# Kernel tuning notes

Hardware: AMD Instinct MI355X
Metric: run time of the kernel (lower is better)

## Reference

```python
import jax, jax.numpy as jnp
import numpy as np

VOCAB, EMB, UNITS, B, S = 32000, 256, 512, 32, 512


def _lstm_scan(x_bse, h0, c0, W, U, b):
    """Keras-order LSTM (gates i,f,g,o). x_bse: [B,S,E]. Returns (out [B,S,U], hT, cT)."""
    # Precompute input projections for all timesteps: [B,S,4U] -> [S,B,4U]
    zx = jnp.einsum('bse,eu->bsu', x_bse, W) + b
    zx = jnp.swapaxes(zx, 0, 1)

    def step(carry, zt):
        h, c = carry
        z = zt + h @ U  # [B,4U]
        i, f, g, o = jnp.split(z, 4, axis=-1)
        i = jax.nn.sigmoid(i)
        f = jax.nn.sigmoid(f)
        g = jnp.tanh(g)
        o = jax.nn.sigmoid(o)
        c = f * c + i * g
        h = o * jnp.tanh(c)
        return (h, c), h

    (hT, cT), hs = jax.lax.scan(step, (h0, c0), zx)
    return jnp.swapaxes(hs, 0, 1), hT, cT


def setup_inputs() -> dict:
    key = jax.random.key(0)
    ks = jax.random.split(key, 8)
    g = 0.05
    inp = {
        'x': jax.random.randint(ks[0], (B, S), 0, VOCAB),
        'fh': jnp.zeros((B, UNITS), jnp.float32),
        'fc': jnp.zeros((B, UNITS), jnp.float32),
        'bh': jnp.zeros((B, UNITS), jnp.float32),
        'bc': jnp.zeros((B, UNITS), jnp.float32),
        'emb': jax.random.normal(ks[1], (VOCAB, EMB), jnp.float32) * g,
        'Wf': jax.random.normal(ks[2], (EMB, 4 * UNITS), jnp.float32) * g,
        'Uf': jax.random.normal(ks[3], (UNITS, 4 * UNITS), jnp.float32) * g,
        'bf': jnp.zeros((4 * UNITS,), jnp.float32),
        'Wb': jax.random.normal(ks[4], (EMB, 4 * UNITS), jnp.float32) * g,
        'Ub': jax.random.normal(ks[5], (UNITS, 4 * UNITS), jnp.float32) * g,
        'bb': jnp.zeros((4 * UNITS,), jnp.float32),
    }
    return inp


def reference(x, fh, fc, bh, bc, emb, Wf, Uf, bf, Wb, Ub, bb):
    xe = emb[x]  # [B,S,E] embedding lookup
    # Forward direction
    out_f, fhT, fcT = _lstm_scan(xe, fh, fc, Wf, Uf, bf)
    # Backward direction: process reversed sequence, then re-reverse outputs
    out_b_rev, bhT, bcT = _lstm_scan(xe[:, ::-1, :], bh, bc, Wb, Ub, bb)
    out_b = out_b_rev[:, ::-1, :]
    output = jnp.concatenate([out_f, out_b], axis=-1)  # [B,S,2U]
    return output, fhT, fcT, bhT, bcT
```

## Files before the change

### kernel.cpp

```cpp
#include <hip/hip_runtime.h>

#define SEQ   512
#define BATCH 32
#define EMBD  256
#define UNITS 512
#define G4    2048
#define NW1   128
#define NW2   32
#define UPW   16
#define HSTR  520
#define NTHR  512

typedef short  short8 __attribute__((ext_vector_type(8)));
typedef float  f32x4  __attribute__((ext_vector_type(4)));
typedef unsigned int u32x4 __attribute__((ext_vector_type(4)));
typedef unsigned int u32x2 __attribute__((ext_vector_type(2)));

static constexpr unsigned long long ZX2_OFF   = 0ull;
static constexpr unsigned long long ZX2_BYTES = 2ull * SEQ * NW1 * BATCH * 16 * 2;
static constexpr unsigned long long HB_OFF    = ZX2_OFF + ZX2_BYTES;
static constexpr unsigned long long HB_BYTES  = 2ull * SEQ * BATCH * UNITS * 2;
static constexpr unsigned long long FLG_OFF   = HB_OFF + HB_BYTES;
static constexpr unsigned long long FLG_BYTES = 4096;
static constexpr unsigned long long SF_OFF    = FLG_OFF + FLG_BYTES;
static constexpr unsigned long long SF_BYTES  = 2ull * SEQ * NW2 * 4;

__device__ __forceinline__ unsigned short f2bf(float f) {
  unsigned int u = __float_as_uint(f);
  u = (u + 0x7FFFu + ((u >> 16) & 1u)) >> 16;
  return (unsigned short)u;
}
__device__ __forceinline__ float bf2f(unsigned short s) {
  return __uint_as_float(((unsigned int)s) << 16);
}
__device__ __forceinline__ unsigned sent2(unsigned w) {
  return (unsigned)(((w & 0xFFFFu) == 0xFFFFu) | ((w >> 16) == 0xFFFFu));
}
__device__ __forceinline__ unsigned chk4(u32x4 g) {
  return sent2(g[0]) | sent2(g[1]) | sent2(g[2]) | sent2(g[3]);
}

__global__ __launch_bounds__(256)
void k_zx(const int* __restrict__ x, const float* __restrict__ emb,
          const float* __restrict__ Wf, const float* __restrict__ bf,
          const float* __restrict__ Wb, const float* __restrict__ bb,
          unsigned short* __restrict__ zx2)
{
  const int nb  = blockIdx.x;
  const int mb  = blockIdx.y;
  const int dir = blockIdx.z;
  const float* __restrict__ W    = dir ? Wb : Wf;
  const float* __restrict__ bias = dir ? bb : bf;
  const int tid = threadIdx.x;
  const int M0 = mb * 64, N0 = nb * 64;

  __shared__ __align__(16) float Ast[32][68];
  __shared__ __align__(16) float Bs [32][68];
  __shared__ int tok[64];

  if (tid < 64) {
    int m = M0 + tid;
    int t = m >> 5, b = m & 31;
    int s = dir ? (SEQ - 1 - t) : t;
    tok[tid] = x[b * SEQ + s];
  }

  float acc[4][4];
  #pragma unroll
  for (int r = 0; r < 4; ++r)
    #pragma unroll
    for (int c = 0; c < 4; ++c) acc[r][c] = 0.f;

  const int mq = tid >> 4, nq = tid & 15;

  for (int kb = 0; kb < 8; ++kb) {
    __syncthreads();
    {
      int m = tid >> 2, q = tid & 3;
      const float* src = emb + (size_t)tok[m] * EMBD + kb * 32 + q * 8;
      float4 v0 = *(const float4*)src;
      float4 v1 = *(const float4*)(src + 4);
      int k0 = q * 8;
      Ast[k0+0][m] = v0.x; Ast[k0+1][m] = v0.y; Ast[k0+2][m] = v0.z; Ast[k0+3][m] = v0.w;
      Ast[k0+4][m] = v1.x; Ast[k0+5][m] = v1.y; Ast[k0+6][m] = v1.z; Ast[k0+7][m] = v1.w;
    }
    {
      int k = tid >> 3, q = tid & 7;
      const float* src = W + (size_t)(kb*32 + k) * G4 + N0 + q * 8;
      float4 w0 = *(const float4*)src;
      float4 w1 = *(const float4*)(src + 4);
      *(float4*)&Bs[k][q*8]     = w0;
      *(float4*)&Bs[k][q*8 + 4] = w1;
    }
    __syncthreads();
    #pragma unroll 8
    for (int k = 0; k < 32; ++k) {
      float4 a  = *(const float4*)&Ast[k][mq*4];
      float4 bv = *(const float4*)&Bs[k][nq*4];
      acc[0][0] += a.x*bv.x; acc[0][1] += a.x*bv.y; acc[0][2] += a.x*bv.z; acc[0][3] += a.x*bv.w;
      acc[1][0] += a.y*bv.x; acc[1][1] += a.y*bv.y; acc[1][2] += a.y*bv.z; acc[1][3] += a.y*bv.w;
      acc[2][0] += a.z*bv.x; acc[2][1] += a.z*bv.y; acc[2][2] += a.z*bv.z; acc[2][3] += a.z*bv.w;
      acc[3][0] += a.w*bv.x; acc[3][1] += a.w*bv.y; acc[3][2] += a.w*bv.z; acc[3][3] += a.w*bv.w;
    }
  }

  float4 bs4 = *(const float4*)(bias + N0 + nq*4);
  const int g = N0 >> 9;
  const int u = (N0 & 511) + nq * 4;
  const int w = u >> 2;
  #pragma unroll
  for (int r = 0; r < 4; ++r) {
    int m = M0 + mq*4 + r;
    int t = m >> 5, b = m & 31;
    unsigned short p0 = f2bf(acc[r][0] + bs4.x);
    unsigned short p1 = f2bf(acc[r][1] + bs4.y);
    unsigned short p2 = f2bf(acc[r][2] + bs4.z);
    unsigned short p3 = f2bf(acc[r][3] + bs4.w);
    uint2 pk;
    pk.x = (unsigned)p0 | ((unsigned)p1 << 16);
    pk.y = (unsigned)p2 | ((unsigned)p3 << 16);
    size_t off = ((((size_t)dir*SEQ + t)*NW1 + w)*BATCH + b)*16 + g*4;
    *(uint2*)(zx2 + off) = pk;
  }
}

__global__ __launch_bounds__(NTHR, 2)
void k_rec2(const float* __restrict__ fh, const float* __restrict__ fc,
            const float* __restrict__ bh, const float* __restrict__ bc,
            const float* __restrict__ Uf, const float* __restrict__ Ub,
            const unsigned short* __restrict__ zx2,
            unsigned short* __restrict__ hring_all,
            int* __restrict__ claim, int* __restrict__ sflag,
            float* __restrict__ out)
{
  const int tid = threadIdx.x;
  __shared__ int s_slot, s_loc;

  if (tid == 0) {
    unsigned xcc;
    asm volatile("s_getreg_b32 %0, hwreg(HW_REG_XCC_ID)" : "=s"(xcc));
    int slot = -1;
    if (xcc < 2) {
      int base = (int)xcc * NW2;
      for (int i = 0; i < NW2 && slot < 0; ++i)
        if (atomicCAS(&claim[base + i], 0, 1) == 0) slot = base + i;
    }
    if (slot < 0) {
      for (int sp = 0; sp < 96; ++sp) __builtin_amdgcn_s_sleep(8);
      for (int i = 0; i < 2 * NW2 && slot < 0; ++i)
        if (atomicCAS(&claim[i], 0, 1) == 0) slot = i;
    }
    s_slot = slot;
    s_loc  = (slot >= 0 && (unsigned)(slot >> 5) == xcc) ? 1 : 0;
  }
  __syncthreads();
  const int slot = s_slot;
  if (slot < 0) return;
  const int loc = s_loc;
  const int dir = slot >> 5;
  const int w   = slot & (NW2 - 1);
  const int u0  = w * UPW;
  const int l   = tid & 63;
  const int wid = tid >> 6;
  const int mt  = wid & 1;
  const int ct  = wid >> 1;

  const float* __restrict__ U  = dir ? Ub : Uf;
  const float* __restrict__ h0 = dir ? bh : fh;
  const float* __restrict__ c0 = dir ? bc : fc;

  __shared__ __align__(16) unsigned short hs[BATCH * HSTR];
  __shared__ __align__(16) float obuf[2][8][BATCH][16];

  unsigned short* __restrict__ hring = hring_all + (size_t)dir * SEQ * BATCH * UNITS;
  int* __restrict__ flg = sflag + (size_t)dir * SEQ * NW2;
  const unsigned short* __restrict__ zxd =
      zx2 + ((size_t)dir * SEQ) * (NW1 * BATCH * 16);

  const int krow = (l >> 4) * 8;
  const size_t gcol = (size_t)((l & 15) >> 2) * 512 + u0 + ct * 4 + (l & 3);
  short8 uhi[16], ulo[16];
  #pragma unroll
  for (int s = 0; s < 16; ++s) {
    const float* up = U + (size_t)(s * 32 + krow) * G4 + gcol;
    short8 hi8, lo8;
    #pragma unroll
    for (int j = 0; j < 8; ++j) {
      float uv = up[(size_t)j * G4];
      unsigned short h16 = f2bf(uv);
      float rem = uv - bf2f(h16);
      hi8[j] = (short)h16;
      lo8[j] = (short)f2bf(rem);
    }
    uhi[s] = hi8; ulo[s] = lo8;
  }

  float c_old[4];
  #pragma unroll
  for (int r = 0; r < 4; ++r) {
    int b_r = 16 * mt + (l >> 4) * 4 + r;
    c_old[r] = c0[(size_t)b_r * UNITS + u0 + ct * 4 + (l & 3)];
  }

  {
    int r = tid >> 4, cq = tid & 15;
    const float* src = h0 + (size_t)r * UNITS;
    #pragma unroll
    for (int i = 0; i < 4; ++i) {
      int c = i * 16 + cq;
      float4 v0 = *(const float4*)(src + c * 8);
      float4 v1 = *(const float4*)(src + c * 8 + 4);
      short8 pk;
      pk[0]=(short)f2bf(v0.x); pk[1]=(short)f2bf(v0.y);
      pk[2]=(short)f2bf(v0.z); pk[3]=(short)f2bf(v0.w);
      pk[4]=(short)f2bf(v1.x); pk[5]=(short)f2bf(v1.y);
      pk[6]=(short)f2bf(v1.z); pk[7]=(short)f2bf(v1.w);
      *(short8*)(&hs[r * HSTR + c * 8]) = pk;
    }
  }
  __syncthreads();

  const int arow  = 16 * mt + (l & 15);
  const unsigned short* hsrow = hs + arow * HSTR;
  const int agrp0 = l >> 4;
  const int sr = tid >> 4, scq = tid & 15;
  unsigned short* const hs_dst = hs + sr * HSTR + scq * 8;
  const bool isg = ((l & 15) >> 2) == 2;
  const float An = isg ? 2.f : 1.f;
  const float Cn = isg ? -1.f : 0.f;
  const float Bn = isg ? -2.f : -1.f;
  const size_t ZXT = (size_t)NW1 * BATCH * 16;
  const size_t zbase = ((size_t)(4 * w + ct) * BATCH + 16 * mt + (l >> 4) * 4) * 16
                       + ((l & 15) >> 2) * 4 + (l & 3);
  const int bj = wid, bb_ = (tid >> 1) & 31, uqp = tid & 1;

  unsigned short zx_cur[4];
  #pragma unroll
  for (int r = 0; r < 4; ++r) zx_cur[r] = zxd[zbase + r * 16];

  for (int t = 0; t < SEQ; ++t) {
    if (t > 0) {
      if (wid == 0) {
        const int* fpl = flg + (size_t)(t - 1) * NW2 + (l & 31);
        unsigned v; int guard = 0;
        for (;;) {
          if ((guard & 3) == 3)
            asm volatile("global_load_dword %0, %1, off sc0 sc1\n\ts_waitcnt vmcnt(0)"
                         : "=v"(v) : "v"(fpl) : "memory");
          else
            asm volatile("global_load_dword %0, %1, off sc0\n\ts_waitcnt vmcnt(0)"
                         : "=v"(v) : "v"(fpl) : "memory");
          __builtin_amdgcn_sched_barrier(0);
          if (__ballot(v != 0) == ~0ull || ++guard >= (1 << 20)) break;
          __builtin_amdgcn_s_sleep(1);
        }
      }
      __syncthreads();
      const unsigned short* src =
          hring + ((size_t)(t - 1) * BATCH + sr) * UNITS + scq * 8;
      u32x4 g0, g1, g2, g3;
      asm volatile("global_load_dwordx4 %0, %1, off sc0"            : "=&v"(g0) : "v"(src) : "memory");
      asm volatile("global_load_dwordx4 %0, %1, off offset:256 sc0" : "=&v"(g1) : "v"(src) : "memory");
      asm volatile("global_load_dwordx4 %0, %1, off offset:512 sc0" : "=&v"(g2) : "v"(src) : "memory");
      asm volatile("global_load_dwordx4 %0, %1, off offset:768 sc0" : "=&v"(g3) : "v"(src) : "memory");
      asm volatile("s_waitcnt vmcnt(0)" : "+v"(g0), "+v"(g1), "+v"(g2), "+v"(g3));
      __builtin_amdgcn_sched_barrier(0);
      unsigned b0 = chk4(g0), b1 = chk4(g1), b2 = chk4(g2), b3 = chk4(g3);
      int guard = 0;
      while ((b0 | b1 | b2 | b3) && ++guard < (1 << 20)) {
        __builtin_amdgcn_s_sleep(1);
        if (guard & 1) {
          if (b0) asm volatile("global_load_dwordx4 %0, %1, off sc0 sc1"            : "=&v"(g0) : "v"(src) : "memory");
          if (b1) asm volatile("global_load_dwordx4 %0, %1, off offset:256 sc0 sc1" : "=&v"(g1) : "v"(src) : "memory");
          if (b2) asm volatile("global_load_dwordx4 %0, %1, off offset:512 sc0 sc1" : "=&v"(g2) : "v"(src) : "memory");
          if (b3) asm volatile("global_load_dwordx4 %0, %1, off offset:768 sc0 sc1" : "=&v"(g3) : "v"(src) : "memory");
        } else {
          if (b0) asm volatile("global_load_dwordx4 %0, %1, off sc0"            : "=&v"(g0) : "v"(src) : "memory");
          if (b1) asm volatile("global_load_dwordx4 %0, %1, off offset:256 sc0" : "=&v"(g1) : "v"(src) : "memory");
          if (b2) asm volatile("global_load_dwordx4 %0, %1, off offset:512 sc0" : "=&v"(g2) : "v"(src) : "memory");
          if (b3) asm volatile("global_load_dwordx4 %0, %1, off offset:768 sc0" : "=&v"(g3) : "v"(src) : "memory");
        }
        asm volatile("s_waitcnt vmcnt(0)" : "+v"(g0), "+v"(g1), "+v"(g2), "+v"(g3));
        __builtin_amdgcn_sched_barrier(0);
        b0 = chk4(g0); b1 = chk4(g1); b2 = chk4(g2); b3 = chk4(g3);
      }
      *(u32x4*)(hs_dst      ) = g0;
      *(u32x4*)(hs_dst + 128) = g1;
      *(u32x4*)(hs_dst + 256) = g2;
      *(u32x4*)(hs_dst + 384) = g3;

      if ((t & 7) == 0 && t >= 8) {
        int tb = t - 8, bank = ((t - 8) >> 3) & 1;
        int tj = tb + bj;
        int sidx = dir ? (SEQ - 1 - tj) : tj;
        const f32x4* sp = (const f32x4*)&obuf[bank][bj][bb_][uqp * 8];
        f32x4 v0 = sp[0];
        f32x4 v1 = sp[1];
        float* dst = out + ((size_t)bb_ * SEQ + sidx) * 1024 + dir * 512 + u0 + uqp * 8;
        __builtin_nontemporal_store(v0, (f32x4*)dst);
        __builtin_nontemporal_store(v1, (f32x4*)(dst + 4));
      }
      __builtin_amdgcn_sched_barrier(0);
    }

    unsigned short zx_nxt[4] = {0, 0, 0, 0};
    if (t + 1 < SEQ) {
      #pragma unroll
      for (int r = 0; r < 4; ++r)
        zx_nxt[r] = zxd[(size_t)(t + 1) * ZXT + zbase + r * 16];
    }
    __builtin_amdgcn_sched_barrier(0);
    if (t > 0) __syncthreads();

    f32x4 accA = {0.f, 0.f, 0.f, 0.f};
    f32x4 accB = {0.f, 0.f, 0.f, 0.f};
    #pragma unroll
    for (int s = 0; s < 16; ++s) {
      short8 a = *(const short8*)(hsrow + (4 * s + agrp0) * 8);
      accA = __builtin_amdgcn_mfma_f32_16x16x32_bf16(a, uhi[s], accA, 0, 0, 0);
      accB = __builtin_amdgcn_mfma_f32_16x16x32_bf16(a, ulo[s], accB, 0, 0, 0);
    }

    float vv[4];
    #pragma unroll
    for (int r = 0; r < 4; ++r) {
      float z = accA[r] + accB[r] + bf2f(zx_cur[r]);
      float e = __expf(Bn * z);
      vv[r] = An * __builtin_amdgcn_rcpf(1.f + e) + Cn;
    }
    float hn[4], cn[4];
    unsigned pk0[4], pk1[4];
    #pragma unroll
    for (int r = 0; r < 4; ++r) {
      float wv = __shfl_xor(vv[r], 8);
      float x1 = __shfl_xor(vv[r], 4);
      float x2 = __shfl_xor(wv,    4);
      cn[r] = x1 * c_old[r] + vv[r] * wv;
      c_old[r] = cn[r];
      float e2 = __expf(-2.f * cn[r]);
      float th = 2.f * __builtin_amdgcn_rcpf(1.f + e2) - 1.f;
      hn[r] = x2 * th;
      unsigned hb = (unsigned)f2bf(hn[r]);
      unsigned d  = (hb & 0xFFFFu) | (__shfl_xor((int)hb, 1) << 16);
      unsigned d2 = (unsigned)__shfl_xor((int)d, 2);
      pk0[r] = d; pk1[r] = d2;
    }

    if (t < SEQ - 1) {
      if ((l & 15) == 0) {
        #pragma unroll
        for (int r = 0; r < 4; ++r) {
          int b_r = 16 * mt + (l >> 4) * 4 + r;
          unsigned short* dst = hring + ((size_t)t * BATCH + b_r) * UNITS + u0 + ct * 4;
          u32x2 pk; pk[0] = pk0[r]; pk[1] = pk1[r];
          if (loc)
            asm volatile("global_store_dwordx2 %0, %1, off sc0"
                         :: "v"(dst), "v"(pk) : "memory");
          else
            asm volatile("global_store_dwordx2 %0, %1, off sc0 sc1"
                         :: "v"(dst), "v"(pk) : "memory");
        }
      }
      __builtin_amdgcn_sched_barrier(0);
      if (tid == 0) {
        int* fdst = flg + (size_t)t * NW2 + w;
        unsigned one = 1u;
        if (loc)
          asm volatile("global_store_dword %0, %1, off sc0"
                       :: "v"(fdst), "v"(one) : "memory");
        else
          asm volatile("global_store_dword %0, %1, off sc0 sc1"
                       :: "v"(fdst), "v"(one) : "memory");
      }
    }
    __builtin_amdgcn_sched_barrier(0);

    if ((l & 15) < 4) {
      int jj = t & 7, bank = (t >> 3) & 1;
      #pragma unroll
      for (int r = 0; r < 4; ++r)
        obuf[bank][jj][16 * mt + (l >> 4) * 4 + r][ct * 4 + (l & 3)] = hn[r];
      if (t == SEQ - 1) {
        size_t base = (size_t)BATCH * SEQ * 1024;
        #pragma unroll
        for (int r = 0; r < 4; ++r) {
          int b_r = 16 * mt + (l >> 4) * 4 + r;
          size_t o1 = base + (size_t)(2*dir  ) * BATCH * UNITS + (size_t)b_r * UNITS + u0 + ct * 4 + (l & 3);
          size_t o2 = base + (size_t)(2*dir+1) * BATCH * UNITS + (size_t)b_r * UNITS + u0 + ct * 4 + (l & 3);
          __builtin_nontemporal_store(hn[r], &out[o1]);
          __builtin_nontemporal_store(cn[r], &out[o2]);
        }
      }
    }

    #pragma unroll
    for (int r = 0; r < 4; ++r) zx_cur[r] = zx_nxt[r];
  }

  __syncthreads();
  {
    int tb = SEQ - 8, bank = ((SEQ - 8) >> 3) & 1;
    int tj = tb + bj;
    int sidx = dir ? (SEQ - 1 - tj) : tj;
    const f32x4* sp = (const f32x4*)&obuf[bank][bj][bb_][uqp * 8];
    f32x4 v0 = sp[0];
    f32x4 v1 = sp[1];
    float* dst = out + ((size_t)bb_ * SEQ + sidx) * 1024 + dir * 512 + u0 + uqp * 8;
    __builtin_nontemporal_store(v0, (f32x4*)dst);
    __builtin_nontemporal_store(v1, (f32x4*)(dst + 4));
  }
}

extern "C" void kernel_launch(void* const* d_in, const int* in_sizes, int n_in,
                              void* d_out, int out_size, void* d_ws, size_t ws_size,
                              hipStream_t stream)
{
  const int*   x   = (const int*)  d_in[0];
  const float* fh  = (const float*)d_in[1];
  const float* fc  = (const float*)d_in[2];
  const float* bh  = (const float*)d_in[3];
  const float* bc  = (const float*)d_in[4];
  const float* emb = (const float*)d_in[5];
  const float* Wf  = (const float*)d_in[6];
  const float* Uf  = (const float*)d_in[7];
  const float* bf  = (const float*)d_in[8];
  const float* Wb  = (const float*)d_in[9];
  const float* Ub  = (const float*)d_in[10];
  const float* bb  = (const float*)d_in[11];
  float* out = (float*)d_out;

  if (ws_size < SF_OFF + SF_BYTES) return;

  unsigned short* zx2   = (unsigned short*)((char*)d_ws + ZX2_OFF);
  unsigned short* hring = (unsigned short*)((char*)d_ws + HB_OFF);
  int*            claim = (int*)((char*)d_ws + FLG_OFF);
  int*            sflag = (int*)((char*)d_ws + SF_OFF);

  hipMemsetAsync(hring, 0xFF, HB_BYTES, stream);
  hipMemsetAsync(claim, 0, FLG_BYTES + SF_BYTES, stream);
  k_zx  <<<dim3(32, 256, 2), 256, 0, stream>>>(x, emb, Wf, bf, Wb, bb, zx2);
  k_rec2<<<dim3(256), NTHR, 0, stream>>>(fh, fc, bh, bc, Uf, Ub, zx2, hring, claim, sflag, out);
}
```

Before: 1.963 ms.

## Split recurrent workgroups by batch half so each syncs with only 16 peers

Changes the recurrent kernel's work split from 32 unit-slices × full batch to 16 unit-slices × 2 batch halves per direction. Each workgroup then covers 32 units for 16 rows, so it polls 16 peer flags instead of 32 and loads half as much h per step. The aim is to cut cross-workgroup sync and h-ring traffic on the serial critical path. In exchange, the flag store now waits on vmcnt and a full __syncthreads, which adds latency per step. Each workgroup also keeps 32 columns of U in registers.

```diff
diff --git a/kernel.cpp b/kernel.cpp
--- a/kernel.cpp
+++ b/kernel.cpp
@@ -6,8 +6,9 @@
 #define UNITS 512
 #define G4    2048
 #define NW1   128
-#define NW2   32
-#define UPW   16
+#define NWD   32
+#define UPW   32
+#define RPW   16
 #define HSTR  520
 #define NTHR  512
 
@@ -23,7 +24,7 @@
 static constexpr unsigned long long FLG_OFF   = HB_OFF + HB_BYTES;
 static constexpr unsigned long long FLG_BYTES = 4096;
 static constexpr unsigned long long SF_OFF    = FLG_OFF + FLG_BYTES;
-static constexpr unsigned long long SF_BYTES  = 2ull * SEQ * NW2 * 4;
+static constexpr unsigned long long SF_BYTES  = 2ull * SEQ * NWD * 4;
 
 __device__ __forceinline__ unsigned short f2bf(float f) {
   unsigned int u = __float_as_uint(f);
@@ -141,13 +142,13 @@
     asm volatile("s_getreg_b32 %0, hwreg(HW_REG_XCC_ID)" : "=s"(xcc));
     int slot = -1;
     if (xcc < 2) {
-      int base = (int)xcc * NW2;
-      for (int i = 0; i < NW2 && slot < 0; ++i)
+      int base = (int)xcc * NWD;
+      for (int i = 0; i < NWD && slot < 0; ++i)
         if (atomicCAS(&claim[base + i], 0, 1) == 0) slot = base + i;
     }
     if (slot < 0) {
       for (int sp = 0; sp < 96; ++sp) __builtin_amdgcn_s_sleep(8);
-      for (int i = 0; i < 2 * NW2 && slot < 0; ++i)
+      for (int i = 0; i < 2 * NWD && slot < 0; ++i)
         if (atomicCAS(&claim[i], 0, 1) == 0) slot = i;
     }
     s_slot = slot;
@@ -158,27 +159,29 @@
   if (slot < 0) return;
   const int loc = s_loc;
   const int dir = slot >> 5;
-  const int w   = slot & (NW2 - 1);
-  const int u0  = w * UPW;
+  const int rg  = (slot >> 4) & 1;
+  const int ug  = slot & 15;
+  const int u0  = ug * UPW;
+  const int r0  = rg * RPW;
   const int l   = tid & 63;
   const int wid = tid >> 6;
-  const int mt  = wid & 1;
-  const int ct  = wid >> 1;
+  const int ct  = wid;
 
   const float* __restrict__ U  = dir ? Ub : Uf;
   const float* __restrict__ h0 = dir ? bh : fh;
   const float* __restrict__ c0 = dir ? bc : fc;
 
-  __shared__ __align__(16) unsigned short hs[BATCH * HSTR];
-  __shared__ __align__(16) float obuf[2][8][BATCH][16];
+  __shared__ __align__(16) unsigned short hs[RPW * HSTR];
+  __shared__ __align__(16) float obuf[2][8][RPW][36];
 
   unsigned short* __restrict__ hring = hring_all + (size_t)dir * SEQ * BATCH * UNITS;
-  int* __restrict__ flg = sflag + (size_t)dir * SEQ * NW2;
+  int* __restrict__ flg = sflag + (size_t)dir * SEQ * NWD;
   const unsigned short* __restrict__ zxd =
       zx2 + ((size_t)dir * SEQ) * (NW1 * BATCH * 16);
 
+  const int gate = (l & 15) >> 2;
   const int krow = (l >> 4) * 8;
-  const size_t gcol = (size_t)((l & 15) >> 2) * 512 + u0 + ct * 4 + (l & 3);
+  const size_t gcol = (size_t)gate * 512 + u0 + ct * 4 + (l & 3);
   short8 uhi[16], ulo[16];
   #pragma unroll
   for (int s = 0; s < 16; ++s) {
@@ -198,16 +201,16 @@
   float c_old[4];
   #pragma unroll
   for (int r = 0; r < 4; ++r) {
-    int b_r = 16 * mt + (l >> 4) * 4 + r;
+    int b_r = r0 + (l >> 4) * 4 + r;
     c_old[r] = c0[(size_t)b_r * UNITS + u0 + ct * 4 + (l & 3)];
   }
 
   {
-    int r = tid >> 4, cq = tid & 15;
-    const float* src = h0 + (size_t)r * UNITS;
-    #pragma unroll
-    for (int i = 0; i < 4; ++i) {
-      int c = i * 16 + cq;
+    int r = tid >> 5, cq = tid & 31;
+    const float* src = h0 + (size_t)(r0 + r) * UNITS;
+    #pragma unroll
+    for (int i = 0; i < 2; ++i) {
+      int c = i * 32 + cq;
       float4 v0 = *(const float4*)(src + c * 8);
       float4 v1 = *(const float4*)(src + c * 8 + 4);
       short8 pk;
@@ -220,19 +223,19 @@
   }
   __syncthreads();
 
-  const int arow  = 16 * mt + (l & 15);
+  const int arow  = l & 15;
   const unsigned short* hsrow = hs + arow * HSTR;
   const int agrp0 = l >> 4;
-  const int sr = tid >> 4, scq = tid & 15;
-  unsigned short* const hs_dst = hs + sr * HSTR + scq * 8;
-  const bool isg = ((l & 15) >> 2) == 2;
+  const int sr = tid >> 5, scq = tid & 31;
+  unsigned short* const hs_dst = hs + sr * HSTR + scq * 16;
+  const bool isg = gate == 2;
   const float An = isg ? 2.f : 1.f;
   const float Cn = isg ? -1.f : 0.f;
   const float Bn = isg ? -2.f : -1.f;
   const size_t ZXT = (size_t)NW1 * BATCH * 16;
-  const size_t zbase = ((size_t)(4 * w + ct) * BATCH + 16 * mt + (l >> 4) * 4) * 16
-                       + ((l & 15) >> 2) * 4 + (l & 3);
-  const int bj = wid, bb_ = (tid >> 1) & 31, uqp = tid & 1;
+  const size_t zbase = ((size_t)(8 * ug + ct) * BATCH + r0 + (l >> 4) * 4) * 16
+                       + gate * 4 + (l & 3);
+  const int bj = tid >> 6, brow = (tid >> 2) & 15, buq = tid & 3;
 
   unsigned short zx_cur[4];
   #pragma unroll
@@ -241,7 +244,7 @@
   for (int t = 0; t < SEQ; ++t) {
     if (t > 0) {
       if (wid == 0) {
-        const int* fpl = flg + (size_t)(t - 1) * NW2 + (l & 31);
+        const int* fpl = flg + (size_t)(t - 1) * NWD + rg * 16 + (l & 15);
         unsigned v; int guard = 0;
         for (;;) {
           if ((guard & 3) == 3)
@@ -257,46 +260,38 @@
       }
       __syncthreads();
       const unsigned short* src =
-          hring + ((size_t)(t - 1) * BATCH + sr) * UNITS + scq * 8;
-      u32x4 g0, g1, g2, g3;
-      asm volatile("global_load_dwordx4 %0, %1, off sc0"            : "=&v"(g0) : "v"(src) : "memory");
-      asm volatile("global_load_dwordx4 %0, %1, off offset:256 sc0" : "=&v"(g1) : "v"(src) : "memory");
-      asm volatile("global_load_dwordx4 %0, %1, off offset:512 sc0" : "=&v"(g2) : "v"(src) : "memory");
-      asm volatile("global_load_dwordx4 %0, %1, off offset:768 sc0" : "=&v"(g3) : "v"(src) : "memory");
-      asm volatile("s_waitcnt vmcnt(0)" : "+v"(g0), "+v"(g1), "+v"(g2), "+v"(g3));
+          hring + ((size_t)(t - 1) * BATCH + r0 + sr) * UNITS + scq * 16;
+      u32x4 g0, g1;
+      asm volatile("global_load_dwordx4 %0, %1, off sc0"           : "=&v"(g0) : "v"(src) : "memory");
+      asm volatile("global_load_dwordx4 %0, %1, off offset:16 sc0" : "=&v"(g1) : "v"(src) : "memory");
+      asm volatile("s_waitcnt vmcnt(0)" : "+v"(g0), "+v"(g1));
       __builtin_amdgcn_sched_barrier(0);
-      unsigned b0 = chk4(g0), b1 = chk4(g1), b2 = chk4(g2), b3 = chk4(g3);
+      unsigned b0 = chk4(g0), b1 = chk4(g1);
       int guard = 0;
-      while ((b0 | b1 | b2 | b3) && ++guard < (1 << 20)) {
+      while ((b0 | b1) && ++guard < (1 << 20)) {
         __builtin_amdgcn_s_sleep(1);
         if (guard & 1) {
-          if (b0) asm volatile("global_load_dwordx4 %0, %1, off sc0 sc1"            : "=&v"(g0) : "v"(src) : "memory");
-          if (b1) asm volatile("global_load_dwordx4 %0, %1, off offset:256 sc0 sc1" : "=&v"(g1) : "v"(src) : "memory");
-          if (b2) asm volatile("global_load_dwordx4 %0, %1, off offset:512 sc0 sc1" : "=&v"(g2) : "v"(src) : "memory");
-          if (b3) asm volatile("global_load_dwordx4 %0, %1, off offset:768 sc0 sc1" : "=&v"(g3) : "v"(src) : "memory");
+          if (b0) asm volatile("global_load_dwordx4 %0, %1, off sc0 sc1"           : "=&v"(g0) : "v"(src) : "memory");
+          if (b1) asm volatile("global_load_dwordx4 %0, %1, off offset:16 sc0 sc1" : "=&v"(g1) : "v"(src) : "memory");
         } else {
-          if (b0) asm volatile("global_load_dwordx4 %0, %1, off sc0"            : "=&v"(g0) : "v"(src) : "memory");
-          if (b1) asm volatile("global_load_dwordx4 %0, %1, off offset:256 sc0" : "=&v"(g1) : "v"(src) : "memory");
-          if (b2) asm volatile("global_load_dwordx4 %0, %1, off offset:512 sc0" : "=&v"(g2) : "v"(src) : "memory");
-          if (b3) asm volatile("global_load_dwordx4 %0, %1, off offset:768 sc0" : "=&v"(g3) : "v"(src) : "memory");
+          if (b0) asm volatile("global_load_dwordx4 %0, %1, off sc0"           : "=&v"(g0) : "v"(src) : "memory");
+          if (b1) asm volatile("global_load_dwordx4 %0, %1, off offset:16 sc0" : "=&v"(g1) : "v"(src) : "memory");
         }
-        asm volatile("s_waitcnt vmcnt(0)" : "+v"(g0), "+v"(g1), "+v"(g2), "+v"(g3));
+        asm volatile("s_waitcnt vmcnt(0)" : "+v"(g0), "+v"(g1));
         __builtin_amdgcn_sched_barrier(0);
-        b0 = chk4(g0); b1 = chk4(g1); b2 = chk4(g2); b3 = chk4(g3);
-      }
-      *(u32x4*)(hs_dst      ) = g0;
-      *(u32x4*)(hs_dst + 128) = g1;
-      *(u32x4*)(hs_dst + 256) = g2;
-      *(u32x4*)(hs_dst + 384) = g3;
+        b0 = chk4(g0); b1 = chk4(g1);
+      }
+      *(u32x4*)(hs_dst    ) = g0;
+      *(u32x4*)(hs_dst + 8) = g1;
 
       if ((t & 7) == 0 && t >= 8) {
         int tb = t - 8, bank = ((t - 8) >> 3) & 1;
         int tj = tb + bj;
         int sidx = dir ? (SEQ - 1 - tj) : tj;
-        const f32x4* sp = (const f32x4*)&obuf[bank][bj][bb_][uqp * 8];
+        const f32x4* sp = (const f32x4*)&obuf[bank][bj][brow][buq * 8];
         f32x4 v0 = sp[0];
         f32x4 v1 = sp[1];
-        float* dst = out + ((size_t)bb_ * SEQ + sidx) * 1024 + dir * 512 + u0 + uqp * 8;
+        float* dst = out + ((size_t)(r0 + brow) * SEQ + sidx) * 1024 + dir * 512 + u0 + buq * 8;
         __builtin_nontemporal_store(v0, (f32x4*)dst);
         __builtin_nontemporal_store(v1, (f32x4*)(dst + 4));
       }
@@ -350,7 +345,7 @@
       if ((l & 15) == 0) {
         #pragma unroll
         for (int r = 0; r < 4; ++r) {
-          int b_r = 16 * mt + (l >> 4) * 4 + r;
+          int b_r = r0 + (l >> 4) * 4 + r;
           unsigned short* dst = hring + ((size_t)t * BATCH + b_r) * UNITS + u0 + ct * 4;
           u32x2 pk; pk[0] = pk0[r]; pk[1] = pk1[r];
           if (loc)
@@ -361,9 +356,10 @@
                          :: "v"(dst), "v"(pk) : "memory");
         }
       }
-      __builtin_amdgcn_sched_barrier(0);
+      asm volatile("s_waitcnt vmcnt(0)" ::: "memory");
+      __syncthreads();
       if (tid == 0) {
-        int* fdst = flg + (size_t)t * NW2 + w;
+        int* fdst = flg + (size_t)t * NWD + rg * 16 + ug;
         unsigned one = 1u;
         if (loc)
           asm volatile("global_store_dword %0, %1, off sc0"
@@ -379,12 +375,12 @@
       int jj = t & 7, bank = (t >> 3) & 1;
       #pragma unroll
       for (int r = 0; r < 4; ++r)
-        obuf[bank][jj][16 * mt + (l >> 4) * 4 + r][ct * 4 + (l & 3)] = hn[r];
+        obuf[bank][jj][(l >> 4) * 4 + r][ct * 4 + (l & 3)] = hn[r];
       if (t == SEQ - 1) {
         size_t base = (size_t)BATCH * SEQ * 1024;
         #pragma unroll
         for (int r = 0; r < 4; ++r) {
-          int b_r = 16 * mt + (l >> 4) * 4 + r;
+          int b_r = r0 + (l >> 4) * 4 + r;
           size_t o1 = base + (size_t)(2*dir  ) * BATCH * UNITS + (size_t)b_r * UNITS + u0 + ct * 4 + (l & 3);
           size_t o2 = base + (size_t)(2*dir+1) * BATCH * UNITS + (size_t)b_r * UNITS + u0 + ct * 4 + (l & 3);
           __builtin_nontemporal_store(hn[r], &out[o1]);
@@ -402,10 +398,10 @@
     int tb = SEQ - 8, bank = ((SEQ - 8) >> 3) & 1;
     int tj = tb + bj;
     int sidx = dir ? (SEQ - 1 - tj) : tj;
-    const f32x4* sp = (const f32x4*)&obuf[bank][bj][bb_][uqp * 8];
+    const f32x4* sp = (const f32x4*)&obuf[bank][bj][brow][buq * 8];
     f32x4 v0 = sp[0];
     f32x4 v1 = sp[1];
-    float* dst = out + ((size_t)bb_ * SEQ + sidx) * 1024 + dir * 512 + u0 + uqp * 8;
+    float* dst = out + ((size_t)(r0 + brow) * SEQ + sidx) * 1024 + dir * 512 + u0 + buq * 8;
     __builtin_nontemporal_store(v0, (f32x4*)dst);
     __builtin_nontemporal_store(v1, (f32x4*)(dst + 4));
   }
```

Result: faster. 1.887 ms, median of 7 (-3.9%).
